# Kernel tuning notes

Measured on AMD Instinct MI355X. Metric: run time of the kernel, lower is better.

Reference implementation:

```python
import jax, jax.numpy as jnp
import numpy as np

WS = 7        # window_size
NH = 12       # num_heads
HD = 32       # head_dim
SCALE = HD ** -0.5


def _rel_pos_index(ws: int) -> np.ndarray:
    # Static [N, N] index into the (2ws-1)^2 relative position bias table.
    coords = np.stack(np.meshgrid(np.arange(ws), np.arange(ws), indexing='ij'))
    coords = coords.reshape(2, -1)                       # [2, N]
    rel = coords[:, :, None] - coords[:, None, :]        # [2, N, N]
    rel = rel.transpose(1, 2, 0).copy()                  # [N, N, 2]
    rel[:, :, 0] += ws - 1
    rel[:, :, 1] += ws - 1
    rel[:, :, 0] *= 2 * ws - 1
    return rel.sum(-1)                                   # [N, N]

_REL_IDX = jnp.asarray(_rel_pos_index(WS))


def setup_inputs() -> dict:
    key = jax.random.key(0)
    ks = jax.random.split(key, 7)
    BW, N, C = 2048, WS * WS, 384
    nW = 64
    return {
        'x': jax.random.normal(ks[0], (BW, N, C), jnp.float32),
        'mask': jax.random.normal(ks[1], (nW, N, N), jnp.float32),
        'qkv_w': jax.random.normal(ks[2], (3 * C, C), jnp.float32) * 0.02,
        'qkv_b': jax.random.normal(ks[3], (3 * C,), jnp.float32) * 0.02,
        'proj_w': jax.random.normal(ks[4], (C, C), jnp.float32) * 0.02,
        'proj_b': jax.random.normal(ks[5], (C,), jnp.float32) * 0.02,
        'bias_table': jax.random.normal(ks[6], ((2 * WS - 1) ** 2, NH), jnp.float32) * 0.02,
    }


def reference(x, mask, qkv_w, qkv_b, proj_w, proj_b, bias_table):
    BW, N, C = x.shape
    # qkv projection: [BW, N, 3, H, hd]
    qkv = (x @ qkv_w.T + qkv_b).reshape(BW, N, 3, NH, HD)
    qkv = jnp.transpose(qkv, (2, 0, 3, 1, 4))            # [3, BW, H, N, hd]
    q, k, v = qkv[0], qkv[1], qkv[2]
    attn = jnp.einsum('bhnd,bhmd->bhnm', q, k) * SCALE   # [BW, H, N, N]
    # gathered relative position bias: [N, N, H] -> [H, N, N]
    bias = bias_table[_REL_IDX]                          # [N, N, H]
    attn = attn + jnp.transpose(bias, (2, 0, 1))[None]
    # shifted-window mask add: [nW, N, N] broadcast over batch and heads
    nW = mask.shape[0]
    attn = attn.reshape(BW // nW, nW, NH, N, N) + mask[None, :, None]
    attn = attn.reshape(BW, NH, N, N)
    attn = jax.nn.softmax(attn, axis=-1)
    out = jnp.einsum('bhnm,bhmd->bhnd', attn, v)         # [BW, H, N, hd]
    out = jnp.transpose(out, (0, 2, 1, 3)).reshape(BW, N, C)
    return out @ proj_w.T + proj_b
```

## Files before the change

kernel.cpp:

```cpp
#include <hip/hip_runtime.h>

typedef __attribute__((ext_vector_type(4))) float f32x4;
typedef __attribute__((ext_vector_type(8))) short s16x8;

#define MFMA16(a, b, c) __builtin_amdgcn_mfma_f32_16x16x32_bf16(a, b, c, 0, 0, 0)

static __device__ __forceinline__ unsigned short f2b(float f) {
  unsigned int u = __float_as_uint(f);
  u += 0x7fff + ((u >> 16) & 1);
  return (unsigned short)(u >> 16);
}

static __device__ __forceinline__ void gload_lds16(const unsigned short* g, unsigned short* l) {
  __builtin_amdgcn_global_load_lds(
      (const __attribute__((address_space(1))) unsigned int*)g,
      (__attribute__((address_space(3))) unsigned int*)l, 16, 0, 0);
}

#define BW    2048
#define NTOK  49
#define TPAD  64
#define CDIM  384
#define NHEAD 12
#define HDIM  32
#define NWIN  64
#define MROWS (BW * NTOK)
#define MPAD  (BW * TPAD)
#define SCALE 0.17677669529663687f
#define QKP   ((size_t)BW * NHEAD * TPAD * HDIM)

#define OFF_XP   ((size_t)0)
#define OFF_Q    ((size_t)100663296)
#define OFF_K    ((size_t)201326592)
#define OFF_QW   ((size_t)301989888)
#define OFF_PW   ((size_t)302874624)
#define OFF_COMB ((size_t)303169536)

__global__ __launch_bounds__(256) void cast_pad(const float* __restrict__ x,
                                                unsigned short* __restrict__ xp) {
  const int i = blockIdx.x * 256 + threadIdx.x;
  const int prow = i / 48;
  const int cc = i - prow * 48;
  const int t = prow & 63;
  s16x8 o;
  if (t < NTOK) {
    const int srow = (prow >> 6) * NTOK + t;
    const float4* s = (const float4*)(x + (size_t)srow * CDIM + cc * 8);
    float4 f0 = s[0], f1 = s[1];
    o[0] = f2b(f0.x); o[1] = f2b(f0.y); o[2] = f2b(f0.z); o[3] = f2b(f0.w);
    o[4] = f2b(f1.x); o[5] = f2b(f1.y); o[6] = f2b(f1.z); o[7] = f2b(f1.w);
  } else {
#pragma unroll
    for (int j = 0; j < 8; ++j) o[j] = 0;
  }
  *(s16x8*)(xp + (size_t)prow * CDIM + cc * 8) = o;
}

__global__ __launch_bounds__(256) void cast_kernel(const float* __restrict__ src,
                                                   unsigned short* __restrict__ dst, int n4) {
  int i = blockIdx.x * 256 + threadIdx.x;
  if (i >= n4) return;
  float4 f = ((const float4*)src)[i];
  ushort4 o;
  o.x = f2b(f.x); o.y = f2b(f.y); o.z = f2b(f.z); o.w = f2b(f.w);
  ((ushort4*)dst)[i] = o;
}

__global__ __launch_bounds__(256) void build_comb(const float* __restrict__ mask,
                                                  const float* __restrict__ bias_table,
                                                  float* __restrict__ comb) {
  int idx = blockIdx.x * 256 + threadIdx.x;
  if (idx >= NWIN * NHEAD * NTOK * NTOK) return;
  int ij = idx % (NTOK * NTOK);
  int wh = idx / (NTOK * NTOK);
  int h = wh % NHEAD;
  int w = wh / NHEAD;
  int i = ij / NTOK, j = ij % NTOK;
  int yi = i / 7, xi = i % 7, yj = j / 7, xj = j % 7;
  int rel = (yi - yj + 6) * 13 + (xi - xj + 6);
  comb[idx] = mask[w * (NTOK * NTOK) + ij] + bias_table[rel * NHEAD + h];
}

#define CSTR 136
template <int MODE, int MT>
__global__ __launch_bounds__(256) void gemm_bt(const unsigned short* __restrict__ A,
                                               const unsigned short* __restrict__ Bt,
                                               const float* __restrict__ bias,
                                               void* __restrict__ Cv,
                                               unsigned short* __restrict__ vtb,
                                               int N, int K) {
  __shared__ __align__(16) unsigned short smem[MODE == 2 ? 128 * CSTR : 8192];
  unsigned short* As = smem;
  unsigned short* Bs = smem + 4096;
  const int tid = threadIdx.x;
  const int lane = tid & 63;
  const int wave = tid >> 6;
  const int lr = lane & 15, lg = lane >> 4;
  const int wm = (wave >> 1) * 64, wn = (wave & 1) * 64;
  const int lin = blockIdx.x;
  const int tm = lin % MT;
  const int tn = lin / MT;
  const size_t tileM = (size_t)tm * 128;
  const size_t tileN = (size_t)tn * 128;

  const unsigned short* Ab = A + tileM * K;
  const unsigned short* Bb = Bt + tileN * K;

  const int c0 = tid, c1 = tid + 256;
  const size_t a0 = (size_t)(c0 >> 2) * K + (c0 & 3) * 8;
  const size_t a1 = (size_t)(c1 >> 2) * K + (c1 & 3) * 8;

  f32x4 acc[4][4] = {};

  for (int k0 = 0; k0 < K; k0 += 32) {
    gload_lds16(Ab + a0 + k0, As + c0 * 8);
    gload_lds16(Ab + a1 + k0, As + c1 * 8);
    gload_lds16(Bb + a0 + k0, Bs + c0 * 8);
    gload_lds16(Bb + a1 + k0, Bs + c1 * 8);
    __syncthreads();
    s16x8 af[4], bf[4];
#pragma unroll
    for (int mt = 0; mt < 4; ++mt)
      af[mt] = *(const s16x8*)&As[(wm + mt * 16 + lr) * 32 + lg * 8];
#pragma unroll
    for (int nt = 0; nt < 4; ++nt)
      bf[nt] = *(const s16x8*)&Bs[(wn + nt * 16 + lr) * 32 + lg * 8];
#pragma unroll
    for (int mt = 0; mt < 4; ++mt)
#pragma unroll
      for (int nt = 0; nt < 4; ++nt)
        acc[mt][nt] = MFMA16(af[mt], bf[nt], acc[mt][nt]);
    __syncthreads();
  }

  if (MODE == 0) {
    float* Cf = (float*)Cv;
#pragma unroll
    for (int nt = 0; nt < 4; ++nt) {
      const size_t gcol = tileN + wn + nt * 16 + lr;
      const float bv = bias[gcol];
#pragma unroll
      for (int mt = 0; mt < 4; ++mt)
#pragma unroll
        for (int r = 0; r < 4; ++r) {
          const size_t grow = tileM + wm + mt * 16 + lg * 4 + r;
          Cf[grow * (size_t)N + gcol] = acc[mt][nt][r] + bv;
        }
    }
  } else {
    float bv[4];
#pragma unroll
    for (int nt = 0; nt < 4; ++nt) bv[nt] = bias[tileN + wn + nt * 16 + lr];
#pragma unroll
    for (int mt = 0; mt < 4; ++mt)
#pragma unroll
      for (int r = 0; r < 4; ++r) {
        const int row = wm + mt * 16 + lg * 4 + r;
#pragma unroll
        for (int nt = 0; nt < 4; ++nt)
          smem[row * CSTR + wn + nt * 16 + lr] = f2b(acc[mt][nt][r] + bv[nt]);
      }
    __syncthreads();

    const int which = tn / 3;
    if (which < 2) {
      unsigned short* qko = (unsigned short*)Cv + (size_t)which * QKP;
#pragma unroll
      for (int i = 0; i < 8; ++i) {
        const int c = i * 256 + tid;
        const int row = c >> 4, cg = c & 15;
        s16x8 v = *(const s16x8*)&smem[row * CSTR + cg * 8];
        const int grow = (int)tileM + row;
        const int b = grow >> 6, t = grow & 63;
        const int col = (int)tileN + cg * 8 - which * CDIM;
        const int hh = col >> 5, d0 = col & 31;
        *(s16x8*)(qko + (((size_t)b * NHEAD + hh) * TPAD + t) * HDIM + d0) = v;
      }
    } else {
#pragma unroll
      for (int i = 0; i < 8; ++i) {
        const int c = i * 256 + tid;
        const int col = c >> 4, w = (c >> 3) & 1, tc = c & 7;
        s16x8 v;
#pragma unroll
        for (int j = 0; j < 8; ++j) v[j] = smem[(w * 64 + tc * 8 + j) * CSTR + col];
        const int b = tm * 2 + w;
        const int cc = (int)tileN + col - 2 * CDIM;
        const int hh = cc >> 5, d = cc & 31;
        *(s16x8*)(vtb + (((size_t)b * NHEAD + hh) * HDIM + d) * TPAD + tc * 8) = v;
      }
    }
  }
}

#define PSTR 72
__global__ __launch_bounds__(64) void attn_kernel(const unsigned short* __restrict__ q,
                                                  const unsigned short* __restrict__ k,
                                                  const unsigned short* __restrict__ vt,
                                                  const float* __restrict__ comb,
                                                  unsigned short* __restrict__ out) {
  __shared__ __align__(16) unsigned short Pt[64 * PSTR];
  const int b = blockIdx.x;
  const int h = blockIdx.y;
  const int lane = threadIdx.x;
  const int lr = lane & 15, lg = lane >> 4;
  const size_t bh = (size_t)b * NHEAD + h;
  const unsigned short* qb = q + bh * (TPAD * HDIM);
  const unsigned short* kb = k + bh * (TPAD * HDIM);
  const unsigned short* vb = vt + bh * (HDIM * TPAD);

  s16x8 qf[4], kf[4];
#pragma unroll
  for (int mt = 0; mt < 4; ++mt) {
    const int off = (mt * 16 + lr) * HDIM + lg * 8;
    qf[mt] = *(const s16x8*)(qb + off);
    kf[mt] = *(const s16x8*)(kb + off);
  }

  f32x4 S[4][4] = {};
#pragma unroll
  for (int mt = 0; mt < 4; ++mt)
#pragma unroll
    for (int nt = 0; nt < 4; ++nt)
      S[mt][nt] = MFMA16(qf[mt], kf[nt], S[mt][nt]);

  const float* cb = comb + ((size_t)(b & 63) * NHEAD + h) * (NTOK * NTOK);

#pragma unroll
  for (int mt = 0; mt < 4; ++mt) {
#pragma unroll
    for (int r = 0; r < 4; ++r) {
      const int row = mt * 16 + lg * 4 + r;
      const bool rowok = row < NTOK;
      float sv[4];
      float mx = -1e30f;
#pragma unroll
      for (int nt = 0; nt < 4; ++nt) {
        const int col = nt * 16 + lr;
        float s;
        if (col < NTOK)
          s = rowok ? S[mt][nt][r] * SCALE + cb[row * NTOK + col] : 0.0f;
        else
          s = -1e30f;
        sv[nt] = s;
        mx = fmaxf(mx, s);
      }
#pragma unroll
      for (int off = 8; off; off >>= 1) mx = fmaxf(mx, __shfl_xor(mx, off, 16));
      float sum = 0.f;
#pragma unroll
      for (int nt = 0; nt < 4; ++nt) {
        float e = exp2f((sv[nt] - mx) * 1.4426950408889634f);
        sv[nt] = e;
        sum += e;
      }
#pragma unroll
      for (int off = 8; off; off >>= 1) sum += __shfl_xor(sum, off, 16);
      const float inv = 1.0f / sum;
#pragma unroll
      for (int nt = 0; nt < 4; ++nt)
        Pt[row * PSTR + nt * 16 + lr] = f2b(sv[nt] * inv);
    }
  }
  __syncthreads();

  f32x4 O[4][2] = {};
#pragma unroll
  for (int ks = 0; ks < 2; ++ks) {
    s16x8 pf[4], vf[2];
#pragma unroll
    for (int mt = 0; mt < 4; ++mt)
      pf[mt] = *(const s16x8*)&Pt[(mt * 16 + lr) * PSTR + ks * 32 + lg * 8];
#pragma unroll
    for (int n2 = 0; n2 < 2; ++n2)
      vf[n2] = *(const s16x8*)(vb + (n2 * 16 + lr) * TPAD + ks * 32 + lg * 8);
#pragma unroll
    for (int mt = 0; mt < 4; ++mt)
#pragma unroll
      for (int n2 = 0; n2 < 2; ++n2)
        O[mt][n2] = MFMA16(pf[mt], vf[n2], O[mt][n2]);
  }

  unsigned short* ob = out + (size_t)b * NTOK * CDIM + h * HDIM;
#pragma unroll
  for (int mt = 0; mt < 4; ++mt)
#pragma unroll
    for (int r = 0; r < 4; ++r) {
      const int row = mt * 16 + lg * 4 + r;
      if (row < NTOK) {
#pragma unroll
        for (int n2 = 0; n2 < 2; ++n2)
          ob[(size_t)row * CDIM + n2 * 16 + lr] = f2b(O[mt][n2][r]);
      }
    }
}

extern "C" void kernel_launch(void* const* d_in, const int* in_sizes, int n_in,
                              void* d_out, int out_size, void* d_ws, size_t ws_size,
                              hipStream_t stream) {
  const float* x          = (const float*)d_in[0];
  const float* mask       = (const float*)d_in[1];
  const float* qkv_w      = (const float*)d_in[2];
  const float* qkv_b      = (const float*)d_in[3];
  const float* proj_w     = (const float*)d_in[4];
  const float* proj_b     = (const float*)d_in[5];
  const float* bias_table = (const float*)d_in[6];
  float* out = (float*)d_out;
  char* ws = (char*)d_ws;

  unsigned short* xp   = (unsigned short*)(ws + OFF_XP);
  unsigned short* qb   = (unsigned short*)(ws + OFF_Q);
  unsigned short* kb   = (unsigned short*)(ws + OFF_K);
  unsigned short* qw   = (unsigned short*)(ws + OFF_QW);
  unsigned short* pw   = (unsigned short*)(ws + OFF_PW);
  float* comb          = (float*)(ws + OFF_COMB);
  unsigned short* vtb  = (unsigned short*)d_out;

  cast_pad<<<(MPAD * 48) / 256, 256, 0, stream>>>(x, xp);
  cast_kernel<<<(3 * CDIM * CDIM / 4 + 255) / 256, 256, 0, stream>>>(qkv_w, qw, 3 * CDIM * CDIM / 4);
  cast_kernel<<<(CDIM * CDIM / 4 + 255) / 256, 256, 0, stream>>>(proj_w, pw, CDIM * CDIM / 4);

  {
    int n = NWIN * NHEAD * NTOK * NTOK;
    build_comb<<<(n + 255) / 256, 256, 0, stream>>>(mask, bias_table, comb);
  }

  gemm_bt<2, MPAD / 128><<<(MPAD / 128) * (3 * CDIM / 128), 256, 0, stream>>>(
      xp, qw, qkv_b, qb, vtb, 3 * CDIM, CDIM);

  attn_kernel<<<dim3(BW, NHEAD), 64, 0, stream>>>(qb, kb, vtb, comb, xp);

  gemm_bt<0, MROWS / 128><<<(MROWS / 128) * (CDIM / 128), 256, 0, stream>>>(
      xp, pw, proj_b, out, nullptr, CDIM, CDIM);
}
```

Measured before the change: 758.6 us.

## Swizzle GEMM tile order, fold scale into Q, swap MFMA operands, batch heads per block

The GEMM now walks tiles in grouped chunks (SC row tiles by NT column tiles) for better L2 reuse of A. The QKV GEMM swaps the A/B MFMA operands for Q/K tiles so the epilogue writes packed transposed pairs, folds the softmax scale into Q, and simplifies the V transpose store to vector reads. The attention kernel now handles 4 heads per 256-thread block with per-wave LDS regions and drops the __syncthreads. Without that barrier the P tile is written and read within a single wave, which relies on wave-level ordering of LDS access; padded rows 49..63 of P are left unwritten in the per-wave regions, which overlap.

```diff
diff --git a/kernel.cpp b/kernel.cpp
--- a/kernel.cpp
+++ b/kernel.cpp
@@ -2,6 +2,7 @@
 
 typedef __attribute__((ext_vector_type(4))) float f32x4;
 typedef __attribute__((ext_vector_type(8))) short s16x8;
+typedef __attribute__((ext_vector_type(2))) unsigned int u32x2;
 
 #define MFMA16(a, b, c) __builtin_amdgcn_mfma_f32_16x16x32_bf16(a, b, c, 0, 0, 0)
 
@@ -9,6 +10,9 @@
   unsigned int u = __float_as_uint(f);
   u += 0x7fff + ((u >> 16) & 1);
   return (unsigned short)(u >> 16);
+}
+static __device__ __forceinline__ unsigned int pack2(float a, float b) {
+  return (unsigned int)f2b(a) | ((unsigned int)f2b(b) << 16);
 }
 
 static __device__ __forceinline__ void gload_lds16(const unsigned short* g, unsigned short* l) {
@@ -82,7 +86,7 @@
 }
 
 #define CSTR 136
-template <int MODE, int MT>
+template <int MODE, int MT, int SC, int NT>
 __global__ __launch_bounds__(256) void gemm_bt(const unsigned short* __restrict__ A,
                                                const unsigned short* __restrict__ Bt,
                                                const float* __restrict__ bias,
@@ -97,9 +101,12 @@
   const int wave = tid >> 6;
   const int lr = lane & 15, lg = lane >> 4;
   const int wm = (wave >> 1) * 64, wn = (wave & 1) * 64;
+
   const int lin = blockIdx.x;
-  const int tm = lin % MT;
-  const int tn = lin / MT;
+  const int chunk = lin / (SC * NT);
+  const int rmd = lin - chunk * (SC * NT);
+  const int tn = rmd / SC;
+  const int tm = chunk * SC + (rmd - tn * SC);
   const size_t tileM = (size_t)tm * 128;
   const size_t tileN = (size_t)tn * 128;
 
@@ -109,6 +116,12 @@
   const int c0 = tid, c1 = tid + 256;
   const size_t a0 = (size_t)(c0 >> 2) * K + (c0 & 3) * 8;
   const size_t a1 = (size_t)(c1 >> 2) * K + (c1 & 3) * 8;
+
+  const bool swp = (MODE == 2) && (tn < 6);
+  const unsigned short* srcA = swp ? Bs : As;
+  const unsigned short* srcB = swp ? As : Bs;
+  const int rbA = swp ? wn : wm;
+  const int rbB = swp ? wm : wn;
 
   f32x4 acc[4][4] = {};
 
@@ -120,89 +133,106 @@
     __syncthreads();
     s16x8 af[4], bf[4];
 #pragma unroll
-    for (int mt = 0; mt < 4; ++mt)
-      af[mt] = *(const s16x8*)&As[(wm + mt * 16 + lr) * 32 + lg * 8];
-#pragma unroll
-    for (int nt = 0; nt < 4; ++nt)
-      bf[nt] = *(const s16x8*)&Bs[(wn + nt * 16 + lr) * 32 + lg * 8];
-#pragma unroll
-    for (int mt = 0; mt < 4; ++mt)
-#pragma unroll
-      for (int nt = 0; nt < 4; ++nt)
-        acc[mt][nt] = MFMA16(af[mt], bf[nt], acc[mt][nt]);
+    for (int i = 0; i < 4; ++i)
+      af[i] = *(const s16x8*)&srcA[(rbA + i * 16 + lr) * 32 + lg * 8];
+#pragma unroll
+    for (int j = 0; j < 4; ++j)
+      bf[j] = *(const s16x8*)&srcB[(rbB + j * 16 + lr) * 32 + lg * 8];
+#pragma unroll
+    for (int i = 0; i < 4; ++i)
+#pragma unroll
+      for (int j = 0; j < 4; ++j)
+        acc[i][j] = MFMA16(af[i], bf[j], acc[i][j]);
     __syncthreads();
   }
 
   if (MODE == 0) {
     float* Cf = (float*)Cv;
 #pragma unroll
-    for (int nt = 0; nt < 4; ++nt) {
-      const size_t gcol = tileN + wn + nt * 16 + lr;
+    for (int j = 0; j < 4; ++j) {
+      const size_t gcol = tileN + wn + j * 16 + lr;
       const float bv = bias[gcol];
 #pragma unroll
-      for (int mt = 0; mt < 4; ++mt)
+      for (int i = 0; i < 4; ++i)
 #pragma unroll
         for (int r = 0; r < 4; ++r) {
-          const size_t grow = tileM + wm + mt * 16 + lg * 4 + r;
-          Cf[grow * (size_t)N + gcol] = acc[mt][nt][r] + bv;
+          const size_t grow = tileM + wm + i * 16 + lg * 4 + r;
+          Cf[grow * (size_t)N + gcol] = acc[i][j][r] + bv;
         }
     }
   } else {
-    float bv[4];
-#pragma unroll
-    for (int nt = 0; nt < 4; ++nt) bv[nt] = bias[tileN + wn + nt * 16 + lr];
-#pragma unroll
-    for (int mt = 0; mt < 4; ++mt)
-#pragma unroll
-      for (int r = 0; r < 4; ++r) {
-        const int row = wm + mt * 16 + lg * 4 + r;
-#pragma unroll
-        for (int nt = 0; nt < 4; ++nt)
-          smem[row * CSTR + wn + nt * 16 + lr] = f2b(acc[mt][nt][r] + bv[nt]);
-      }
+    const float scl = (tn < 3) ? SCALE : 1.0f;
+    float4 bb[4];
+    if (swp) {
+#pragma unroll
+      for (int i = 0; i < 4; ++i)
+        bb[i] = *(const float4*)&bias[tileN + rbA + i * 16 + lg * 4];
+    }
+#pragma unroll
+    for (int j = 0; j < 4; ++j) {
+      const int irow = rbB + j * 16 + lr;
+      const float bvr = swp ? 0.0f : bias[tileN + irow];
+#pragma unroll
+      for (int i = 0; i < 4; ++i) {
+        const int icol = rbA + i * 16 + lg * 4;
+        float v0, v1, v2, v3;
+        if (swp) {
+          v0 = (acc[i][j][0] + bb[i].x) * scl;
+          v1 = (acc[i][j][1] + bb[i].y) * scl;
+          v2 = (acc[i][j][2] + bb[i].z) * scl;
+          v3 = (acc[i][j][3] + bb[i].w) * scl;
+        } else {
+          v0 = acc[i][j][0] + bvr; v1 = acc[i][j][1] + bvr;
+          v2 = acc[i][j][2] + bvr; v3 = acc[i][j][3] + bvr;
+        }
+        u32x2 pk; pk[0] = pack2(v0, v1); pk[1] = pack2(v2, v3);
+        *(u32x2*)&smem[irow * CSTR + icol] = pk;
+      }
+    }
     __syncthreads();
 
     const int which = tn / 3;
     if (which < 2) {
-      unsigned short* qko = (unsigned short*)Cv + (size_t)which * QKP;
-#pragma unroll
-      for (int i = 0; i < 8; ++i) {
-        const int c = i * 256 + tid;
+      unsigned short* dst = (unsigned short*)Cv + (size_t)which * QKP;
+#pragma unroll
+      for (int i8 = 0; i8 < 8; ++i8) {
+        const int c = i8 * 256 + tid;
         const int row = c >> 4, cg = c & 15;
         s16x8 v = *(const s16x8*)&smem[row * CSTR + cg * 8];
-        const int grow = (int)tileM + row;
-        const int b = grow >> 6, t = grow & 63;
-        const int col = (int)tileN + cg * 8 - which * CDIM;
-        const int hh = col >> 5, d0 = col & 31;
-        *(s16x8*)(qko + (((size_t)b * NHEAD + hh) * TPAD + t) * HDIM + d0) = v;
+        const int b = (int)(tileM >> 6) + (row >> 6);
+        const int t = row & 63;
+        const int cc = (int)tileN - which * CDIM + cg * 8;
+        const int hh = cc >> 5, d0 = cc & 31;
+        *(s16x8*)(dst + (((size_t)b * NHEAD + hh) * TPAD + t) * HDIM + d0) = v;
       }
     } else {
 #pragma unroll
-      for (int i = 0; i < 8; ++i) {
-        const int c = i * 256 + tid;
-        const int col = c >> 4, w = (c >> 3) & 1, tc = c & 7;
-        s16x8 v;
-#pragma unroll
-        for (int j = 0; j < 8; ++j) v[j] = smem[(w * 64 + tc * 8 + j) * CSTR + col];
-        const int b = tm * 2 + w;
-        const int cc = (int)tileN + col - 2 * CDIM;
+      for (int i8 = 0; i8 < 8; ++i8) {
+        const int c = i8 * 256 + tid;
+        const int row = c >> 4, cg = c & 15;
+        s16x8 v = *(const s16x8*)&smem[row * CSTR + cg * 8];
+        const int cc = (int)tileN - 2 * CDIM + row;
         const int hh = cc >> 5, d = cc & 31;
-        *(s16x8*)(vtb + (((size_t)b * NHEAD + hh) * HDIM + d) * TPAD + tc * 8) = v;
+        const int w = cg >> 3, t0 = (cg & 7) * 8;
+        const int b = (int)(tileM >> 6) + w;
+        *(s16x8*)(vtb + (((size_t)b * NHEAD + hh) * HDIM + d) * TPAD + t0) = v;
       }
     }
   }
 }
 
 #define PSTR 72
-__global__ __launch_bounds__(64) void attn_kernel(const unsigned short* __restrict__ q,
-                                                  const unsigned short* __restrict__ k,
-                                                  const unsigned short* __restrict__ vt,
-                                                  const float* __restrict__ comb,
-                                                  unsigned short* __restrict__ out) {
-  __shared__ __align__(16) unsigned short Pt[64 * PSTR];
+__global__ __launch_bounds__(256) void attn_kernel(const unsigned short* __restrict__ q,
+                                                   const unsigned short* __restrict__ k,
+                                                   const unsigned short* __restrict__ vt,
+                                                   const float* __restrict__ comb,
+                                                   unsigned short* __restrict__ out) {
+  __shared__ __align__(16) unsigned short PtAll[3 * NTOK * PSTR + TPAD * PSTR];
+  const int wave = threadIdx.x >> 6;
+  const int lane = threadIdx.x & 63;
   const int b = blockIdx.x;
-  const int h = blockIdx.y;
-  const int lane = threadIdx.x;
+  const int h = blockIdx.y * 4 + wave;
+  unsigned short* Pt = PtAll + wave * (NTOK * PSTR);
   const int lr = lane & 15, lg = lane >> 4;
   const size_t bh = (size_t)b * NHEAD + h;
   const unsigned short* qb = q + bh * (TPAD * HDIM);
@@ -239,7 +269,7 @@
         const int col = nt * 16 + lr;
         float s;
         if (col < NTOK)
-          s = rowok ? S[mt][nt][r] * SCALE + cb[row * NTOK + col] : 0.0f;
+          s = rowok ? S[mt][nt][r] + cb[row * NTOK + col] : 0.0f;
         else
           s = -1e30f;
         sv[nt] = s;
@@ -257,12 +287,13 @@
 #pragma unroll
       for (int off = 8; off; off >>= 1) sum += __shfl_xor(sum, off, 16);
       const float inv = 1.0f / sum;
-#pragma unroll
-      for (int nt = 0; nt < 4; ++nt)
-        Pt[row * PSTR + nt * 16 + lr] = f2b(sv[nt] * inv);
-    }
-  }
-  __syncthreads();
+      if (rowok) {
+#pragma unroll
+        for (int nt = 0; nt < 4; ++nt)
+          Pt[row * PSTR + nt * 16 + lr] = f2b(sv[nt] * inv);
+      }
+    }
+  }
 
   f32x4 O[4][2] = {};
 #pragma unroll
@@ -325,11 +356,11 @@
     build_comb<<<(n + 255) / 256, 256, 0, stream>>>(mask, bias_table, comb);
   }
 
-  gemm_bt<2, MPAD / 128><<<(MPAD / 128) * (3 * CDIM / 128), 256, 0, stream>>>(
+  gemm_bt<2, MPAD / 128, 64, 9><<<(MPAD / 128) * 9, 256, 0, stream>>>(
       xp, qw, qkv_b, qb, vtb, 3 * CDIM, CDIM);
 
-  attn_kernel<<<dim3(BW, NHEAD), 64, 0, stream>>>(qb, kb, vtb, comb, xp);
-
-  gemm_bt<0, MROWS / 128><<<(MROWS / 128) * (CDIM / 128), 256, 0, stream>>>(
+  attn_kernel<<<dim3(BW, NHEAD / 4), 256, 0, stream>>>(qb, kb, vtb, comb, xp);
+
+  gemm_bt<0, MROWS / 128, 49, 3><<<(MROWS / 128) * 3, 256, 0, stream>>>(
       xp, pw, proj_b, out, nullptr, CDIM, CDIM);
 }
```

Result: faster. 652.7 us (-14.0%).
